# Optimization experiments

Hardware: AMD Instinct MI355X
Metric: run time of the kernel (lower is better)

The kernel has to match this reference:

```python
import jax, jax.numpy as jnp
import numpy as np

ALPHA = 1000.0  # softmin temperature from the original module


def setup_inputs() -> dict:
    key = jax.random.key(0)
    ks = jax.random.split(key, 10)
    B, D, H, E, K = 8192, 784, 256, 32, 512
    s = 0.05  # small init scale to keep activations/distances numerically sane
    return {
        "x": jax.random.normal(ks[0], (B, D), jnp.float32),
        "cluster_reps": jax.random.normal(ks[1], (K, E), jnp.float32),
        "W1": jax.random.normal(ks[2], (D, H), jnp.float32) * s,
        "b1": jnp.zeros((H,), jnp.float32),
        "W2": jax.random.normal(ks[3], (H, E), jnp.float32) * s,
        "b2": jnp.zeros((E,), jnp.float32),
        "W3": jax.random.normal(ks[4], (E, H), jnp.float32) * s,
        "b3": jnp.zeros((H,), jnp.float32),
        "W4": jax.random.normal(ks[5], (H, D), jnp.float32) * s,
        "b4": jnp.zeros((D,), jnp.float32),
    }


def reference(x, cluster_reps, W1, b1, W2, b2, W3, b3, W4, b4):
    # --- autoencoder: 2-layer MLP encoder / decoder ---
    h = jax.nn.relu(x @ W1 + b1)            # [B, H]
    embeddings = h @ W2 + b2                # [B, E]
    h2 = jax.nn.relu(embeddings @ W3 + b3)  # [B, H]
    reconstruction = h2 @ W4 + b4           # [B, D]

    # --- squared distances to cluster reps: [B, K] ---
    diff = embeddings[:, None, :] - cluster_reps[None, :, :]  # [B, K, E]
    distances = jnp.sum(diff * diff, axis=2)                  # [B, K]

    # --- stable softmin-weighted distances ---
    min_dist = jnp.min(distances, axis=1, keepdims=True)       # [B, 1]
    exponentials = jnp.exp(-ALPHA * (distances - min_dist))    # [B, K]
    sum_exponentials = jnp.sum(exponentials, axis=1, keepdims=True)
    weighted_dists = distances * (exponentials / sum_exponentials)

    return (weighted_dists, distances, reconstruction, embeddings)
```

## Files before the change

### kernel.cpp

```cpp
#include <hip/hip_runtime.h>
#include <cstddef>

#define NB 8192
#define ND 784
#define NH 256
#define NE 32
#define NK 512
#define ALPHA_F 1000.0f

typedef _Float16 h8 __attribute__((ext_vector_type(8)));
typedef float f32x4 __attribute__((ext_vector_type(4)));

#define TW1 25
#define TN1 8
#define NBW1 200
#define TW4 8
#define TN4 25
#define NBW4 200
#define NBW2 8
#define NBW3 8

__global__ __launch_bounds__(256)
void prep4_kernel(const float* __restrict__ W1, _Float16* __restrict__ w1thi,
                  _Float16* __restrict__ w1tlo,
                  const float* __restrict__ W4, _Float16* __restrict__ w4thi,
                  _Float16* __restrict__ w4tlo,
                  const float* __restrict__ W2, _Float16* __restrict__ w2thi,
                  _Float16* __restrict__ w2tlo,
                  const float* __restrict__ W3, _Float16* __restrict__ w3thi,
                  _Float16* __restrict__ w3tlo) {
    __shared__ float tile[32][33];
    const int b   = blockIdx.x;
    const int tid = threadIdx.x;

    const float* W; _Float16 *hi, *lo; int K, N, kt, nt;
    if (b < NBW1) {
        W = W1; hi = w1thi; lo = w1tlo; K = ND; N = NH;
        kt = b % TW1; nt = b / TW1;
    } else if (b < NBW1 + NBW4) {
        const int bb = b - NBW1;
        W = W4; hi = w4thi; lo = w4tlo; K = NH; N = ND;
        kt = bb % TW4; nt = bb / TW4;
    } else if (b < NBW1 + NBW4 + NBW2) {
        W = W2; hi = w2thi; lo = w2tlo; K = NH; N = NE;
        kt = b - (NBW1 + NBW4); nt = 0;
    } else {
        W = W3; hi = w3thi; lo = w3tlo; K = NE; N = NH;
        kt = 0; nt = b - (NBW1 + NBW4 + NBW2);
    }
    const int k0 = kt * 32, n0 = nt * 32;
    const int row = tid >> 3, c4 = (tid & 7) * 4;
    #pragma unroll
    for (int j = 0; j < 4; ++j) {
        const int k = k0 + row, n = n0 + c4 + j;
        tile[row][c4 + j] = (k < K && n < N) ? W[(size_t)k * N + n] : 0.f;
    }
    __syncthreads();
    const int n = n0 + row;
    if (n < N) {
        #pragma unroll
        for (int j = 0; j < 4; ++j) {
            const int k = k0 + c4 + j;
            if (k < K) {
                float w = tile[c4 + j][row];
                _Float16 hh = (_Float16)w;
                float r = w - (float)hh;
                hi[(size_t)n * K + k] = hh;
                lo[(size_t)n * K + k] = (_Float16)(r * 2048.0f);
            }
        }
    }
}

#define HSTR 264

__global__ __launch_bounds__(1024, 4)
void mega_kernel(const float* __restrict__ x, const float* __restrict__ reps,
                 const _Float16* __restrict__ w1thi, const _Float16* __restrict__ w1tlo,
                 const _Float16* __restrict__ w2thi, const _Float16* __restrict__ w2tlo,
                 const _Float16* __restrict__ w3thi, const _Float16* __restrict__ w3tlo,
                 const _Float16* __restrict__ w4thi, const _Float16* __restrict__ w4tlo,
                 const float* __restrict__ b1, const float* __restrict__ b2,
                 const float* __restrict__ b3, const float* __restrict__ b4,
                 float* __restrict__ emb_g, float* __restrict__ recon_g,
                 float* __restrict__ dist_g, float* __restrict__ wout_g) {
    __shared__ __align__(16) unsigned char lds[135936];
    _Float16* R0h  = (_Float16*)lds;
    _Float16* sA   = (_Float16*)(lds + 81920);
    _Float16* hP   = (_Float16*)(lds + 92160);
    float*    es   = (float*)(lds + 125952);
    _Float16* eh   = (_Float16*)(lds + 130560);
    _Float16* el   = (_Float16*)(lds + 133120);
    float*    rmin = (float*)(lds + 135680);
    float*    rinv = (float*)(lds + 135808);

    const int tid  = threadIdx.x;
    const int lane = tid & 63;
    const int wv   = tid >> 6;
    const int li   = lane & 15;
    const int kq   = (lane >> 4) * 8;
    const int quad = lane >> 4;
    const int r0   = blockIdx.x * 32;

    const float c1 = 1.0f / 2048.0f;
    const float c2 = c1 * c1;

    {
        _Float16* sBhi = R0h;
        _Float16* sBlo = R0h + 2 * 256 * 40;
        _Float16* sAhi = sA;
        _Float16* sAlo = sA + 2 * 32 * 40;
        const int aro  = tid >> 2;
        const int ak   = (tid & 3) * 8;
        const int brow = tid >> 2;
        const int bk   = (tid & 3) * 8;
        const float*    pA  = x + (size_t)(r0 + aro) * ND;
        const _Float16* pBh = w1thi + (size_t)brow * ND;
        const _Float16* pBl = w1tlo + (size_t)brow * ND;

        float araw[8];
        h8 rbh, rbl;

        auto pf = [&](int s) {
            if (tid < 128) {
                const int k = s * 32 + ak;
                if (k + 8 <= ND) {
                    f32x4 v0 = *(const f32x4*)(pA + k);
                    f32x4 v1 = *(const f32x4*)(pA + k + 4);
                    #pragma unroll
                    for (int j = 0; j < 4; ++j) {
                        araw[j] = v0[j]; araw[4 + j] = v1[j];
                    }
                } else {
                    #pragma unroll
                    for (int j = 0; j < 8; ++j) araw[j] = 0.f;
                }
            }
            const int kb = s * 32 + bk;
            rbh = (kb + 8 <= ND) ? *(const h8*)(pBh + kb) : (h8){};
            rbl = (kb + 8 <= ND) ? *(const h8*)(pBl + kb) : (h8){};
        };
        auto cm = [&](int buf) {
            if (tid < 128) {
                h8 hi, lo;
                #pragma unroll
                for (int j = 0; j < 8; ++j) {
                    float v = araw[j];
                    _Float16 hh = (_Float16)v;
                    hi[j] = hh;
                    lo[j] = (_Float16)((v - (float)hh) * 2048.0f);
                }
                *(h8*)&sAhi[buf * 32 * 40 + aro * 40 + ak] = hi;
                *(h8*)&sAlo[buf * 32 * 40 + aro * 40 + ak] = lo;
            }
            *(h8*)&sBhi[buf * 256 * 40 + brow * 40 + bk] = rbh;
            *(h8*)&sBlo[buf * 256 * 40 + brow * 40 + bk] = rbl;
        };

        pf(0); cm(0); pf(1);
        __syncthreads();

        f32x4 a0[2] = {}, a1[2] = {}, a2[2] = {};
        for (int s = 0; s < 25; ++s) {
            const int buf = s & 1;
            h8 fah[2], fal[2];
            #pragma unroll
            for (int mt = 0; mt < 2; ++mt) {
                const int ao = buf * 32 * 40 + (mt * 16 + li) * 40 + kq;
                fah[mt] = *(const h8*)&sAhi[ao];
                fal[mt] = *(const h8*)&sAlo[ao];
            }
            const int bo = buf * 256 * 40 + (wv * 16 + li) * 40 + kq;
            h8 fbh = *(const h8*)&sBhi[bo];
            h8 fbl = *(const h8*)&sBlo[bo];
            #pragma unroll
            for (int mt = 0; mt < 2; ++mt) {
                a0[mt] = __builtin_amdgcn_mfma_f32_16x16x32_f16(fah[mt], fbh, a0[mt], 0, 0, 0);
                a1[mt] = __builtin_amdgcn_mfma_f32_16x16x32_f16(fah[mt], fbl, a1[mt], 0, 0, 0);
                a1[mt] = __builtin_amdgcn_mfma_f32_16x16x32_f16(fal[mt], fbh, a1[mt], 0, 0, 0);
                a2[mt] = __builtin_amdgcn_mfma_f32_16x16x32_f16(fal[mt], fbl, a2[mt], 0, 0, 0);
            }
            if (s + 1 < 25) { cm((s + 1) & 1); if (s + 2 < 25) pf(s + 2); }
            __syncthreads();
        }
        _Float16* hhi = hP;
        _Float16* hlo = hP + 32 * HSTR;
        const int n = wv * 16 + li;
        const float bv = b1[n];
        #pragma unroll
        for (int mt = 0; mt < 2; ++mt)
            #pragma unroll
            for (int r = 0; r < 4; ++r) {
                const int m = mt * 16 + quad * 4 + r;
                float v = a0[mt][r] + c1 * a1[mt][r] + c2 * a2[mt][r] + bv;
                v = fmaxf(v, 0.f);
                _Float16 t = (_Float16)v;
                hhi[m * HSTR + n] = t;
                hlo[m * HSTR + n] = (_Float16)((v - (float)t) * 2048.0f);
            }
    }
    __syncthreads();

    {
        _Float16* w2h = R0h;
        _Float16* w2l = R0h + 32 * HSTR;
        const int row = tid >> 5, off = (tid & 31) * 8;
        *(h8*)&w2h[row * HSTR + off] = *(const h8*)(w2thi + row * 256 + off);
        *(h8*)&w2l[row * HSTR + off] = *(const h8*)(w2tlo + row * 256 + off);
    }
    __syncthreads();
    if (wv < 4) {
        const int mt = wv >> 1, nt = wv & 1;
        _Float16* hhi = hP;
        _Float16* hlo = hP + 32 * HSTR;
        _Float16* w2h = R0h;
        _Float16* w2l = R0h + 32 * HSTR;
        f32x4 e0 = {}, e1 = {}, e2 = {};
        #pragma unroll
        for (int ks = 0; ks < 8; ++ks) {
            const int k = ks * 32 + kq;
            h8 ah = *(const h8*)&hhi[(mt * 16 + li) * HSTR + k];
            h8 al = *(const h8*)&hlo[(mt * 16 + li) * HSTR + k];
            h8 bh = *(const h8*)&w2h[(nt * 16 + li) * HSTR + k];
            h8 bl = *(const h8*)&w2l[(nt * 16 + li) * HSTR + k];
            e0 = __builtin_amdgcn_mfma_f32_16x16x32_f16(ah, bh, e0, 0, 0, 0);
            e1 = __builtin_amdgcn_mfma_f32_16x16x32_f16(ah, bl, e1, 0, 0, 0);
            e1 = __builtin_amdgcn_mfma_f32_16x16x32_f16(al, bh, e1, 0, 0, 0);
            e2 = __builtin_amdgcn_mfma_f32_16x16x32_f16(al, bl, e2, 0, 0, 0);
        }
        const int col = nt * 16 + li;
        const float bv = b2[col];
        #pragma unroll
        for (int r = 0; r < 4; ++r) {
            const int m = mt * 16 + quad * 4 + r;
            float v = e0[r] + c1 * e1[r] + c2 * e2[r] + bv;
            es[m * 36 + col] = v;
            _Float16 t = (_Float16)v;
            eh[m * 40 + col] = t;
            el[m * 40 + col] = (_Float16)((v - (float)t) * 2048.0f);
            emb_g[(size_t)(r0 + m) * NE + col] = v;
        }
    }
    __syncthreads();

    {
        _Float16* w3h = R0h;
        _Float16* w3l = R0h + 256 * 40;
        const int row = tid >> 2, off = (tid & 3) * 8;
        *(h8*)&w3h[row * 40 + off] = *(const h8*)(w3thi + row * 32 + off);
        *(h8*)&w3l[row * 40 + off] = *(const h8*)(w3tlo + row * 32 + off);
    }
    __syncthreads();
    {
        _Float16* w3h  = R0h;
        _Float16* w3l  = R0h + 256 * 40;
        _Float16* h2h  = hP;
        _Float16* h2l  = hP + 32 * HSTR;
        h8 ah[2], al[2];
        #pragma unroll
        for (int mt = 0; mt < 2; ++mt) {
            ah[mt] = *(const h8*)&eh[(mt * 16 + li) * 40 + kq];
            al[mt] = *(const h8*)&el[(mt * 16 + li) * 40 + kq];
        }
        const int col = wv * 16 + li;
        h8 bh = *(const h8*)&w3h[col * 40 + kq];
        h8 bl = *(const h8*)&w3l[col * 40 + kq];
        const float bv = b3[col];
        #pragma unroll
        for (int mt = 0; mt < 2; ++mt) {
            f32x4 q0 = {}, q1 = {}, q2 = {};
            q0 = __builtin_amdgcn_mfma_f32_16x16x32_f16(ah[mt], bh, q0, 0, 0, 0);
            q1 = __builtin_amdgcn_mfma_f32_16x16x32_f16(ah[mt], bl, q1, 0, 0, 0);
            q1 = __builtin_amdgcn_mfma_f32_16x16x32_f16(al[mt], bh, q1, 0, 0, 0);
            q2 = __builtin_amdgcn_mfma_f32_16x16x32_f16(al[mt], bl, q2, 0, 0, 0);
            #pragma unroll
            for (int r = 0; r < 4; ++r) {
                const int m = mt * 16 + quad * 4 + r;
                float v = q0[r] + c1 * q1[r] + c2 * q2[r] + bv;
                v = fmaxf(v, 0.f);
                _Float16 t = (_Float16)v;
                h2h[m * HSTR + col] = t;
                h2l[m * HSTR + col] = (_Float16)((v - (float)t) * 2048.0f);
            }
        }
    }
    __syncthreads();

    {
        _Float16* sBhi = R0h;
        _Float16* sBlo = R0h + 4 * 128 * 40;
        _Float16* h2h  = hP;
        _Float16* h2l  = hP + 32 * HSTR;
        const int mt  = wv >> 3;
        const int ntw = wv & 7;
        const int brow = tid >> 2;
        const int bk4  = (tid & 3) * 8;
        h8 rbh[2], rbl[2];
        auto pf = [&](int ss) {
            if (tid < 512 && ss < 56) {
                int rg = (ss >> 3) * 128 + brow;
                if (rg > ND - 1) rg = ND - 1;
                const int k = (ss & 7) * 32 + bk4;
                rbh[ss & 1] = *(const h8*)(w4thi + (size_t)rg * NH + k);
                rbl[ss & 1] = *(const h8*)(w4tlo + (size_t)rg * NH + k);
            }
        };
        auto cm = [&](int ss) {
            if (tid < 512 && ss < 56) {
                const int sl = ss & 3;
                *(h8*)&sBhi[sl * 128 * 40 + brow * 40 + bk4] = rbh[ss & 1];
                *(h8*)&sBlo[sl * 128 * 40 + brow * 40 + bk4] = rbl[ss & 1];
            }
        };
        pf(0); pf(1); cm(0); cm(1); pf(2); pf(3);
        __syncthreads();

        f32x4 q0 = {}, q1 = {};
        auto step = [&](int t) {
            const int sl = t & 3, ks = t & 7;
            const int bo = sl * 128 * 40 + (ntw * 16 + li) * 40 + kq;
            h8 fbh = *(const h8*)&sBhi[bo];
            h8 fbl = *(const h8*)&sBlo[bo];
            const int k = ks * 32 + kq;
            h8 ah = *(const h8*)&h2h[(mt * 16 + li) * HSTR + k];
            h8 al = *(const h8*)&h2l[(mt * 16 + li) * HSTR + k];
            q0 = __builtin_amdgcn_mfma_f32_16x16x32_f16(ah, fbh, q0, 0, 0, 0);
            q1 = __builtin_amdgcn_mfma_f32_16x16x32_f16(ah, fbl, q1, 0, 0, 0);
            q1 = __builtin_amdgcn_mfma_f32_16x16x32_f16(al, fbh, q1, 0, 0, 0);
            if (ks == 7) {
                const int n = (t >> 3) * 128 + ntw * 16 + li;
                if (n < ND) {
                    const float bv = b4[n];
                    #pragma unroll
                    for (int r = 0; r < 4; ++r) {
                        const int m = mt * 16 + quad * 4 + r;
                        recon_g[(size_t)(r0 + m) * ND + n] = q0[r] + c1 * q1[r] + bv;
                    }
                }
                q0 = {}; q1 = {};
            }
        };
        for (int ii = 0; ii < 28; ++ii) {
            const int s0 = ii * 2;
            step(s0);
            step(s0 + 1);
            cm(s0 + 2); cm(s0 + 3);
            pf(s0 + 4); pf(s0 + 5);
            __syncthreads();
        }
    }
    __syncthreads();

    {
        float* tr0 = (float*)lds;
        float* tr1 = (float*)(lds + 33280);
        const int half = tid >> 9;
        const int cl   = tid & 511;
        float* trh = half ? tr1 : tr0;
        const int rbase = half * 16;

        const float* rp = reps + (size_t)cl * NE;
        f32x4 rv[8];
        #pragma unroll
        for (int e4 = 0; e4 < 8; ++e4) rv[e4] = ((const f32x4*)rp)[e4];

        float d[16];
        #pragma unroll
        for (int r = 0; r < 16; ++r) {
            float a = 0.f;
            #pragma unroll
            for (int e4 = 0; e4 < 8; ++e4) {
                f32x4 ev = *(const f32x4*)&es[(rbase + r) * 36 + e4 * 4];
                #pragma unroll
                for (int j = 0; j < 4; ++j) {
                    float t = ev[j] - rv[e4][j];
                    a = fmaf(t, t, a);
                }
            }
            d[r] = a;
            trh[r * 520 + cl] = a;
        }
        __syncthreads();
        {
            const int w8 = wv & 7;
            #pragma unroll
            for (int p = 0; p < 2; ++p) {
                const int rl = w8 * 2 + p;
                float m = trh[rl * 520 + lane];
                #pragma unroll
                for (int j = 1; j < 8; ++j)
                    m = fminf(m, trh[rl * 520 + lane + 64 * j]);
                #pragma unroll
                for (int off = 32; off > 0; off >>= 1)
                    m = fminf(m, __shfl_xor(m, off, 64));
                if (lane == 0) rmin[rbase + rl] = m;
            }
        }
        __syncthreads();
        #pragma unroll
        for (int r = 0; r < 16; ++r)
            trh[r * 520 + cl] = expf(-ALPHA_F * (d[r] - rmin[rbase + r]));
        __syncthreads();
        {
            const int w8 = wv & 7;
            #pragma unroll
            for (int p = 0; p < 2; ++p) {
                const int rl = w8 * 2 + p;
                float s = trh[rl * 520 + lane];
                #pragma unroll
                for (int j = 1; j < 8; ++j)
                    s += trh[rl * 520 + lane + 64 * j];
                #pragma unroll
                for (int off = 32; off > 0; off >>= 1)
                    s += __shfl_xor(s, off, 64);
                if (lane == 0) rinv[rbase + rl] = 1.0f / s;
            }
        }
        __syncthreads();
        #pragma unroll
        for (int r = 0; r < 16; ++r) {
            const size_t row = (size_t)(r0 + rbase + r);
            const float ev = trh[r * 520 + cl];
            dist_g[row * NK + cl] = d[r];
            wout_g[row * NK + cl] = d[r] * (ev * rinv[rbase + r]);
        }
    }
}

__global__ __launch_bounds__(256)
void splitw2_kernel(const float* __restrict__ W1, _Float16* __restrict__ w1thi,
                    _Float16* __restrict__ w1tlo,
                    const float* __restrict__ W4, _Float16* __restrict__ w4thi,
                    _Float16* __restrict__ w4tlo) {
    const int b = blockIdx.x;
    const float* W; _Float16 *hi, *lo; int K, N, n;
    if (b < NH) { W = W1; hi = w1thi; lo = w1tlo; K = ND; N = NH; n = b; }
    else        { W = W4; hi = w4thi; lo = w4tlo; K = NH; N = ND; n = b - NH; }
    for (int k = threadIdx.x; k < K; k += 256) {
        float w = W[(size_t)k * N + n];
        _Float16 hh = (_Float16)w;
        float r = w - (float)hh;
        hi[(size_t)n * K + k] = hh;
        lo[(size_t)n * K + k] = (_Float16)(r * 2048.0f);
    }
}

template<int TERMS, bool RELU, bool SPLITA, int MT>
__global__ __launch_bounds__(256)
void mfma_gemm3(const float* __restrict__ Af32,
                const _Float16* __restrict__ Ahi_g,
                const _Float16* __restrict__ Alo_g,
                const _Float16* __restrict__ WThi,
                const _Float16* __restrict__ WTlo,
                const float* __restrict__ bias, float* __restrict__ C,
                int N, int K, int KS) {
    constexpr int BM  = MT * 32;
    constexpr int ACH = BM / 64;
    constexpr int AS  = BM * 40;
    constexpr int BS  = 64 * 40;
    __shared__ __align__(16) _Float16 smem[2 * BM * 40 * 2 + 2 * 64 * 40 * 2];
    _Float16* sAhi = smem;
    _Float16* sAlo = sAhi + 2 * BM * 40;
    _Float16* sBhi = sAlo + 2 * BM * 40;
    _Float16* sBlo = sBhi + 2 * 64 * 40;

    const int tid = threadIdx.x;
    const int bm  = blockIdx.x * BM;
    const int bn  = blockIdx.y * 64;

    const int arow = (ACH == 1) ? (tid >> 2) : (tid >> 1);
    const int ak   = (ACH == 1) ? ((tid & 3) * 8) : ((tid & 1) * 16);
    const int brow = tid >> 2;
    const int bk   = (tid & 3) * 8;

    const float*    pA32 = SPLITA ? Af32 + (size_t)(bm + arow) * K : nullptr;
    const _Float16* pAhi = SPLITA ? nullptr : Ahi_g + (size_t)(bm + arow) * K;
    const _Float16* pAlo = SPLITA ? nullptr : Alo_g + (size_t)(bm + arow) * K;
    int brow_g = bn + brow; if (brow_g > N - 1) brow_g = N - 1;
    const _Float16* pBhi = WThi + (size_t)brow_g * K;
    const _Float16* pBlo = WTlo + (size_t)brow_g * K;

    float araw[ACH * 8];
    h8 rahi[ACH], ralo[ACH];
    h8 rbhi, rblo;

    auto prefetch = [&](int s) {
        #pragma unroll
        for (int c = 0; c < ACH; ++c) {
            const int k = s * 32 + ak + c * 8;
            if (SPLITA) {
                if (k + 8 <= K) {
                    f32x4 v0 = *(const f32x4*)(pA32 + k);
                    f32x4 v1 = *(const f32x4*)(pA32 + k + 4);
                    #pragma unroll
                    for (int j = 0; j < 4; ++j) {
                        araw[c * 8 + j]     = v0[j];
                        araw[c * 8 + 4 + j] = v1[j];
                    }
                } else {
                    #pragma unroll
                    for (int j = 0; j < 8; ++j) araw[c * 8 + j] = 0.f;
                }
            } else {
                rahi[c] = (k + 8 <= K) ? *(const h8*)(pAhi + k) : (h8){};
                ralo[c] = (k + 8 <= K) ? *(const h8*)(pAlo + k) : (h8){};
            }
        }
        const int kb = s * 32 + bk;
        rbhi = (kb + 8 <= K) ? *(const h8*)(pBhi + kb) : (h8){};
        rblo = (kb + 8 <= K) ? *(const h8*)(pBlo + kb) : (h8){};
    };

    auto commit = [&](int buf) {
        #pragma unroll
        for (int c = 0; c < ACH; ++c) {
            h8 hi, lo;
            if (SPLITA) {
                #pragma unroll
                for (int j = 0; j < 8; ++j) {
                    float v = araw[c * 8 + j];
                    _Float16 hh = (_Float16)v;
                    hi[j] = hh;
                    lo[j] = (_Float16)((v - (float)hh) * 2048.0f);
                }
            } else { hi = rahi[c]; lo = ralo[c]; }
            *(h8*)&sAhi[buf * AS + arow * 40 + ak + c * 8] = hi;
            *(h8*)&sAlo[buf * AS + arow * 40 + ak + c * 8] = lo;
        }
        *(h8*)&sBhi[buf * BS + brow * 40 + bk] = rbhi;
        *(h8*)&sBlo[buf * BS + brow * 40 + bk] = rblo;
    };

    prefetch(0);
    commit(0);
    prefetch(1);
    __syncthreads();

    const int lane = tid & 63;
    const int wv   = tid >> 6;
    const int wm   = (wv >> 1) * (MT * 16);
    const int wn   = (wv & 1) * 32;
    const int li   = lane & 15;
    const int kq   = (lane >> 4) * 8;

    f32x4 acc0[MT][2] = {};
    f32x4 acc1[MT][2] = {};
    f32x4 acc2[MT][2] = {};

    for (int s = 0; s < KS; ++s) {
        const int buf = s & 1;
        h8 fahi[MT], falo[MT], fbhi[2], fblo[2];
        #pragma unroll
        for (int mt = 0; mt < MT; ++mt) {
            const int ao = buf * AS + (wm + mt * 16 + li) * 40 + kq;
            fahi[mt] = *(const h8*)&sAhi[ao];
            falo[mt] = *(const h8*)&sAlo[ao];
        }
        #pragma unroll
        for (int nt = 0; nt < 2; ++nt) {
            const int bo = buf * BS + (wn + nt * 16 + li) * 40 + kq;
            fbhi[nt] = *(const h8*)&sBhi[bo];
            fblo[nt] = *(const h8*)&sBlo[bo];
        }
        #pragma unroll
        for (int mt = 0; mt < MT; ++mt)
            #pragma unroll
            for (int nt = 0; nt < 2; ++nt) {
                acc0[mt][nt] = __builtin_amdgcn_mfma_f32_16x16x32_f16(
                    fahi[mt], fbhi[nt], acc0[mt][nt], 0, 0, 0);
                acc1[mt][nt] = __builtin_amdgcn_mfma_f32_16x16x32_f16(
                    fahi[mt], fblo[nt], acc1[mt][nt], 0, 0, 0);
                acc1[mt][nt] = __builtin_amdgcn_mfma_f32_16x16x32_f16(
                    falo[mt], fbhi[nt], acc1[mt][nt], 0, 0, 0);
                if (TERMS == 4)
                    acc2[mt][nt] = __builtin_amdgcn_mfma_f32_16x16x32_f16(
                        falo[mt], fblo[nt], acc2[mt][nt], 0, 0, 0);
            }
        if (s + 1 < KS) {
            commit((s + 1) & 1);
            if (s + 2 < KS) prefetch(s + 2);
        }
        __syncthreads();
    }

    const float c1 = 1.0f / 2048.0f;
    const float c2 = c1 * c1;
    const int quad = lane >> 4;
    #pragma unroll
    for (int nt = 0; nt < 2; ++nt) {
        const int n = bn + wn + nt * 16 + li;
        if (n < N) {
            const float bv = bias[n];
            #pragma unroll
            for (int mt = 0; mt < MT; ++mt) {
                #pragma unroll
                for (int r = 0; r < 4; ++r) {
                    const int m = bm + wm + mt * 16 + quad * 4 + r;
                    float v = acc0[mt][nt][r] + c1 * acc1[mt][nt][r];
                    if (TERMS == 4) v += c2 * acc2[mt][nt][r];
                    v += bv;
                    if (RELU) v = fmaxf(v, 0.f);
                    C[(size_t)m * N + n] = v;
                }
            }
        }
    }
}

__global__ __launch_bounds__(256)
void mid_kernel(const float* __restrict__ h, const float* __restrict__ W2,
                const float* __restrict__ b2, const float* __restrict__ W3,
                const float* __restrict__ b3, float* __restrict__ emb,
                _Float16* __restrict__ h2hi, _Float16* __restrict__ h2lo) {
    __shared__ float es[16][32];
    const int tid = threadIdx.x;
    const int r0  = blockIdx.x * 16;

    #pragma unroll
    for (int half = 0; half < 2; ++half) {
        const int o   = tid + half * 256;
        const int row = o >> 5;
        const int col = o & 31;
        const float* hrow = h + (size_t)(r0 + row) * NH;
        float acc0 = 0.f, acc1 = 0.f;
        #pragma unroll 4
        for (int k = 0; k < NH; k += 4) {
            float4 hv = *(const float4*)(hrow + k);
            acc0 = fmaf(hv.x, W2[(k + 0) * NE + col], acc0);
            acc1 = fmaf(hv.y, W2[(k + 1) * NE + col], acc1);
            acc0 = fmaf(hv.z, W2[(k + 2) * NE + col], acc0);
            acc1 = fmaf(hv.w, W2[(k + 3) * NE + col], acc1);
        }
        float v = acc0 + acc1 + b2[col];
        es[row][col] = v;
        emb[(size_t)r0 * NE + o] = v;
    }
    __syncthreads();

    const int col = tid;
    float acc[16];
    #pragma unroll
    for (int r = 0; r < 16; ++r) acc[r] = 0.f;
    #pragma unroll
    for (int k = 0; k < NE; ++k) {
        float w = W3[k * NH + col];
        #pragma unroll
        for (int r = 0; r < 16; ++r) acc[r] = fmaf(es[r][k], w, acc[r]);
    }
    const float bb = b3[col];
    #pragma unroll
    for (int r = 0; r < 16; ++r) {
        float v = acc[r] + bb;
        v = v > 0.f ? v : 0.f;
        _Float16 hh = (_Float16)v;
        float rr = v - (float)hh;
        h2hi[(size_t)(r0 + r) * NH + col] = hh;
        h2lo[(size_t)(r0 + r) * NH + col] = (_Float16)(rr * 2048.0f);
    }
}

__global__ __launch_bounds__(512, 4)
void dist_kernel(const float* __restrict__ emb, const float* __restrict__ reps,
                 float* __restrict__ dist, float* __restrict__ wout) {
    __shared__ float es[8][32];
    __shared__ float tr[8][520];
    __shared__ float rmin[8];
    __shared__ float rinv[8];

    const int tid = threadIdx.x;
    const int r0  = blockIdx.x * 8;

    if (tid < 256) es[tid >> 5][tid & 31] = emb[(size_t)r0 * NE + tid];

    const float* rp = reps + (size_t)tid * NE;
    f32x4 rv[8];
    #pragma unroll
    for (int e4 = 0; e4 < 8; ++e4) rv[e4] = ((const f32x4*)rp)[e4];
    __syncthreads();

    float d[8];
    #pragma unroll
    for (int r = 0; r < 8; ++r) {
        float a = 0.f;
        #pragma unroll
        for (int e4 = 0; e4 < 8; ++e4) {
            f32x4 ev = *(const f32x4*)&es[r][e4 * 4];
            #pragma unroll
            for (int j = 0; j < 4; ++j) {
                float t = ev[j] - rv[e4][j];
                a = fmaf(t, t, a);
            }
        }
        d[r] = a;
    }

    const int lane = tid & 63;
    const int wv   = tid >> 6;

    #pragma unroll
    for (int r = 0; r < 8; ++r) tr[r][tid] = d[r];
    __syncthreads();
    {
        f32x4 a = *(const f32x4*)&tr[wv][lane * 8];
        f32x4 b = *(const f32x4*)&tr[wv][lane * 8 + 4];
        float m = fminf(fminf(fminf(a[0], a[1]), fminf(a[2], a[3])),
                        fminf(fminf(b[0], b[1]), fminf(b[2], b[3])));
        #pragma unroll
        for (int off = 32; off > 0; off >>= 1)
            m = fminf(m, __shfl_xor(m, off, 64));
        if (lane == 0) rmin[wv] = m;
    }
    __syncthreads();

    float e[8];
    #pragma unroll
    for (int r = 0; r < 8; ++r) {
        e[r] = expf(-ALPHA_F * (d[r] - rmin[r]));
        tr[r][tid] = e[r];
    }
    __syncthreads();
    {
        f32x4 a = *(const f32x4*)&tr[wv][lane * 8];
        f32x4 b = *(const f32x4*)&tr[wv][lane * 8 + 4];
        float s = ((a[0] + a[1]) + (a[2] + a[3])) +
                  ((b[0] + b[1]) + (b[2] + b[3]));
        #pragma unroll
        for (int off = 32; off > 0; off >>= 1)
            s += __shfl_xor(s, off, 64);
        if (lane == 0) rinv[wv] = 1.0f / s;
    }
    __syncthreads();

    #pragma unroll
    for (int r = 0; r < 8; ++r) {
        const size_t row = (size_t)(r0 + r);
        dist[row * NK + tid] = d[r];
        wout[row * NK + tid] = d[r] * (e[r] * rinv[r]);
    }
}

extern "C" void kernel_launch(void* const* d_in, const int* in_sizes, int n_in,
                              void* d_out, int out_size, void* d_ws, size_t ws_size,
                              hipStream_t stream) {
    const float* x    = (const float*)d_in[0];
    const float* reps = (const float*)d_in[1];
    const float* W1   = (const float*)d_in[2];
    const float* b1   = (const float*)d_in[3];
    const float* W2   = (const float*)d_in[4];
    const float* b2   = (const float*)d_in[5];
    const float* W3   = (const float*)d_in[6];
    const float* b3   = (const float*)d_in[7];
    const float* W4   = (const float*)d_in[8];
    const float* b4   = (const float*)d_in[9];

    float* out   = (float*)d_out;
    float* wout  = out;
    float* dist  = out + (size_t)NB * NK;
    float* recon = out + (size_t)2 * NB * NK;
    float* emb   = out + (size_t)2 * NB * NK + (size_t)NB * ND;

    const size_t nW14 = (size_t)ND * NH;
    const size_t nW23 = (size_t)NE * NH;
    const size_t wneed = (4 * nW14 + 4 * nW23) * sizeof(_Float16);

    if (d_ws != nullptr && ws_size >= wneed) {
        _Float16* w1thi = (_Float16*)d_ws;
        _Float16* w1tlo = w1thi + nW14;
        _Float16* w4thi = w1tlo + nW14;
        _Float16* w4tlo = w4thi + nW14;
        _Float16* w2thi = w4tlo + nW14;
        _Float16* w2tlo = w2thi + nW23;
        _Float16* w3thi = w2tlo + nW23;
        _Float16* w3tlo = w3thi + nW23;

        prep4_kernel<<<NBW1 + NBW4 + NBW2 + NBW3, 256, 0, stream>>>(
            W1, w1thi, w1tlo, W4, w4thi, w4tlo,
            W2, w2thi, w2tlo, W3, w3thi, w3tlo);

        mega_kernel<<<NB / 32, 1024, 0, stream>>>(
            x, reps, w1thi, w1tlo, w2thi, w2tlo, w3thi, w3tlo, w4thi, w4tlo,
            b1, b2, b3, b4, emb, recon, dist, wout);
    } else {
        float* h = dist;
        _Float16* h2hi  = (_Float16*)(dist + (size_t)NB * NH);
        _Float16* h2lo  = h2hi + (size_t)NB * NH;
        _Float16* w1thi = (_Float16*)wout;
        _Float16* w1tlo = w1thi + (size_t)NH * ND;
        _Float16* w4thi = w1tlo + (size_t)NH * ND;
        _Float16* w4tlo = w4thi + (size_t)ND * NH;

        splitw2_kernel<<<NH + ND, 256, 0, stream>>>(W1, w1thi, w1tlo,
                                                    W4, w4thi, w4tlo);
        mfma_gemm3<4, true, true, 2><<<dim3(128, 4), 256, 0, stream>>>(
            x, nullptr, nullptr, w1thi, w1tlo, b1, h, NH, ND, 25);
        mid_kernel<<<NB / 16, 256, 0, stream>>>(h, W2, b2, W3, b3,
                                                emb, h2hi, h2lo);
        mfma_gemm3<3, false, false, 4><<<dim3(64, 13), 256, 0, stream>>>(
            nullptr, h2hi, h2lo, w4thi, w4tlo, b4, recon, ND, NH, 8);
        dist_kernel<<<NB / 8, 512, 0, stream>>>(emb, reps, dist, wout);
    }
}
```

Baseline: 162.5 us.

## Replace padded LDS row strides with dense k-blocked 32-wide tiles

Shared-memory tiles switch from padded 40/264-element row strides to unpadded 32-element rows, with the hidden activations and W2 stored in k-blocked 32x32 chunks. The total LDS footprint shrinks and fragment reads become contiguous 1KB spans per wave. This risks different bank-conflict behaviour on scattered epilogue writes and on MFMA fragment loads that the padding previously avoided.

```diff
diff --git a/kernel.cpp b/kernel.cpp
--- a/kernel.cpp
+++ b/kernel.cpp
@@ -72,8 +72,6 @@
     }
 }
 
-#define HSTR 264
-
 __global__ __launch_bounds__(1024, 4)
 void mega_kernel(const float* __restrict__ x, const float* __restrict__ reps,
                  const _Float16* __restrict__ w1thi, const _Float16* __restrict__ w1tlo,
@@ -84,15 +82,14 @@
                  const float* __restrict__ b3, const float* __restrict__ b4,
                  float* __restrict__ emb_g, float* __restrict__ recon_g,
                  float* __restrict__ dist_g, float* __restrict__ wout_g) {
-    __shared__ __align__(16) unsigned char lds[135936];
+    __shared__ __align__(16) unsigned char lds[116480];
     _Float16* R0h  = (_Float16*)lds;
-    _Float16* sA   = (_Float16*)(lds + 81920);
-    _Float16* hP   = (_Float16*)(lds + 92160);
-    float*    es   = (float*)(lds + 125952);
-    _Float16* eh   = (_Float16*)(lds + 130560);
-    _Float16* el   = (_Float16*)(lds + 133120);
-    float*    rmin = (float*)(lds + 135680);
-    float*    rinv = (float*)(lds + 135808);
+    _Float16* sA   = (_Float16*)(lds + 66560);
+    _Float16* hP   = (_Float16*)(lds + 74752);
+    float*    es   = (float*)(lds + 107520);
+    _Float16* eP   = (_Float16*)(lds + 112128);
+    float*    rmin = (float*)(lds + 116224);
+    float*    rinv = (float*)(lds + 116352);
 
     const int tid  = threadIdx.x;
     const int lane = tid & 63;
@@ -107,9 +104,9 @@
 
     {
         _Float16* sBhi = R0h;
-        _Float16* sBlo = R0h + 2 * 256 * 40;
+        _Float16* sBlo = R0h + 2 * 8192;
         _Float16* sAhi = sA;
-        _Float16* sAlo = sA + 2 * 32 * 40;
+        _Float16* sAlo = sA + 2 * 1024;
         const int aro  = tid >> 2;
         const int ak   = (tid & 3) * 8;
         const int brow = tid >> 2;
@@ -150,11 +147,11 @@
                     hi[j] = hh;
                     lo[j] = (_Float16)((v - (float)hh) * 2048.0f);
                 }
-                *(h8*)&sAhi[buf * 32 * 40 + aro * 40 + ak] = hi;
-                *(h8*)&sAlo[buf * 32 * 40 + aro * 40 + ak] = lo;
-            }
-            *(h8*)&sBhi[buf * 256 * 40 + brow * 40 + bk] = rbh;
-            *(h8*)&sBlo[buf * 256 * 40 + brow * 40 + bk] = rbl;
+                *(h8*)&sAhi[buf * 1024 + aro * 32 + ak] = hi;
+                *(h8*)&sAlo[buf * 1024 + aro * 32 + ak] = lo;
+            }
+            *(h8*)&sBhi[buf * 8192 + brow * 32 + bk] = rbh;
+            *(h8*)&sBlo[buf * 8192 + brow * 32 + bk] = rbl;
         };
 
         pf(0); cm(0); pf(1);
@@ -166,11 +163,11 @@
             h8 fah[2], fal[2];
             #pragma unroll
             for (int mt = 0; mt < 2; ++mt) {
-                const int ao = buf * 32 * 40 + (mt * 16 + li) * 40 + kq;
+                const int ao = buf * 1024 + (mt * 16 + li) * 32 + kq;
                 fah[mt] = *(const h8*)&sAhi[ao];
                 fal[mt] = *(const h8*)&sAlo[ao];
             }
-            const int bo = buf * 256 * 40 + (wv * 16 + li) * 40 + kq;
+            const int bo = buf * 8192 + (wv * 16 + li) * 32 + kq;
             h8 fbh = *(const h8*)&sBhi[bo];
             h8 fbl = *(const h8*)&sBlo[bo];
             #pragma unroll
@@ -184,8 +181,9 @@
             __syncthreads();
         }
         _Float16* hhi = hP;
-        _Float16* hlo = hP + 32 * HSTR;
-        const int n = wv * 16 + li;
+        _Float16* hlo = hP + 8192;
+        const int n  = wv * 16 + li;
+        const int nb = n >> 5, nr = n & 31;
         const float bv = b1[n];
         #pragma unroll
         for (int mt = 0; mt < 2; ++mt)
@@ -195,34 +193,36 @@
                 float v = a0[mt][r] + c1 * a1[mt][r] + c2 * a2[mt][r] + bv;
                 v = fmaxf(v, 0.f);
                 _Float16 t = (_Float16)v;
-                hhi[m * HSTR + n] = t;
-                hlo[m * HSTR + n] = (_Float16)((v - (float)t) * 2048.0f);
+                hhi[nb * 1024 + m * 32 + nr] = t;
+                hlo[nb * 1024 + m * 32 + nr] = (_Float16)((v - (float)t) * 2048.0f);
             }
     }
     __syncthreads();
 
     {
         _Float16* w2h = R0h;
-        _Float16* w2l = R0h + 32 * HSTR;
-        const int row = tid >> 5, off = (tid & 31) * 8;
-        *(h8*)&w2h[row * HSTR + off] = *(const h8*)(w2thi + row * 256 + off);
-        *(h8*)&w2l[row * HSTR + off] = *(const h8*)(w2tlo + row * 256 + off);
+        _Float16* w2l = R0h + 8192;
+        const int col = tid >> 5;
+        const int k8  = tid & 31;
+        const int src = col * 256 + k8 * 8;
+        const int dst = (k8 >> 2) * 1024 + col * 32 + (k8 & 3) * 8;
+        *(h8*)&w2h[dst] = *(const h8*)(w2thi + src);
+        *(h8*)&w2l[dst] = *(const h8*)(w2tlo + src);
     }
     __syncthreads();
     if (wv < 4) {
         const int mt = wv >> 1, nt = wv & 1;
         _Float16* hhi = hP;
-        _Float16* hlo = hP + 32 * HSTR;
+        _Float16* hlo = hP + 8192;
         _Float16* w2h = R0h;
-        _Float16* w2l = R0h + 32 * HSTR;
+        _Float16* w2l = R0h + 8192;
         f32x4 e0 = {}, e1 = {}, e2 = {};
         #pragma unroll
         for (int ks = 0; ks < 8; ++ks) {
-            const int k = ks * 32 + kq;
-            h8 ah = *(const h8*)&hhi[(mt * 16 + li) * HSTR + k];
-            h8 al = *(const h8*)&hlo[(mt * 16 + li) * HSTR + k];
-            h8 bh = *(const h8*)&w2h[(nt * 16 + li) * HSTR + k];
-            h8 bl = *(const h8*)&w2l[(nt * 16 + li) * HSTR + k];
+            h8 ah = *(const h8*)&hhi[ks * 1024 + (mt * 16 + li) * 32 + kq];
+            h8 al = *(const h8*)&hlo[ks * 1024 + (mt * 16 + li) * 32 + kq];
+            h8 bh = *(const h8*)&w2h[ks * 1024 + (nt * 16 + li) * 32 + kq];
+            h8 bl = *(const h8*)&w2l[ks * 1024 + (nt * 16 + li) * 32 + kq];
             e0 = __builtin_amdgcn_mfma_f32_16x16x32_f16(ah, bh, e0, 0, 0, 0);
             e1 = __builtin_amdgcn_mfma_f32_16x16x32_f16(ah, bl, e1, 0, 0, 0);
             e1 = __builtin_amdgcn_mfma_f32_16x16x32_f16(al, bh, e1, 0, 0, 0);
@@ -230,14 +230,16 @@
         }
         const int col = nt * 16 + li;
         const float bv = b2[col];
+        _Float16* eh = eP;
+        _Float16* el = eP + 1024;
         #pragma unroll
         for (int r = 0; r < 4; ++r) {
             const int m = mt * 16 + quad * 4 + r;
             float v = e0[r] + c1 * e1[r] + c2 * e2[r] + bv;
             es[m * 36 + col] = v;
             _Float16 t = (_Float16)v;
-            eh[m * 40 + col] = t;
-            el[m * 40 + col] = (_Float16)((v - (float)t) * 2048.0f);
+            eh[m * 32 + col] = t;
+            el[m * 32 + col] = (_Float16)((v - (float)t) * 2048.0f);
             emb_g[(size_t)(r0 + m) * NE + col] = v;
         }
     }
@@ -245,27 +247,30 @@
 
     {
         _Float16* w3h = R0h;
-        _Float16* w3l = R0h + 256 * 40;
-        const int row = tid >> 2, off = (tid & 3) * 8;
-        *(h8*)&w3h[row * 40 + off] = *(const h8*)(w3thi + row * 32 + off);
-        *(h8*)&w3l[row * 40 + off] = *(const h8*)(w3tlo + row * 32 + off);
+        _Float16* w3l = R0h + 8192;
+        const int o = tid * 8;
+        *(h8*)&w3h[o] = *(const h8*)(w3thi + o);
+        *(h8*)&w3l[o] = *(const h8*)(w3tlo + o);
     }
     __syncthreads();
     {
         _Float16* w3h  = R0h;
-        _Float16* w3l  = R0h + 256 * 40;
+        _Float16* w3l  = R0h + 8192;
         _Float16* h2h  = hP;
-        _Float16* h2l  = hP + 32 * HSTR;
+        _Float16* h2l  = hP + 8192;
+        _Float16* eh   = eP;
+        _Float16* el   = eP + 1024;
         h8 ah[2], al[2];
         #pragma unroll
         for (int mt = 0; mt < 2; ++mt) {
-            ah[mt] = *(const h8*)&eh[(mt * 16 + li) * 40 + kq];
-            al[mt] = *(const h8*)&el[(mt * 16 + li) * 40 + kq];
+            ah[mt] = *(const h8*)&eh[(mt * 16 + li) * 32 + kq];
+            al[mt] = *(const h8*)&el[(mt * 16 + li) * 32 + kq];
         }
         const int col = wv * 16 + li;
-        h8 bh = *(const h8*)&w3h[col * 40 + kq];
-        h8 bl = *(const h8*)&w3l[col * 40 + kq];
+        h8 bh = *(const h8*)&w3h[col * 32 + kq];
+        h8 bl = *(const h8*)&w3l[col * 32 + kq];
         const float bv = b3[col];
+        const int cb = col >> 5, cr = col & 31;
         #pragma unroll
         for (int mt = 0; mt < 2; ++mt) {
             f32x4 q0 = {}, q1 = {}, q2 = {};
@@ -279,8 +284,8 @@
                 float v = q0[r] + c1 * q1[r] + c2 * q2[r] + bv;
                 v = fmaxf(v, 0.f);
                 _Float16 t = (_Float16)v;
-                h2h[m * HSTR + col] = t;
-                h2l[m * HSTR + col] = (_Float16)((v - (float)t) * 2048.0f);
+                h2h[cb * 1024 + m * 32 + cr] = t;
+                h2l[cb * 1024 + m * 32 + cr] = (_Float16)((v - (float)t) * 2048.0f);
             }
         }
     }
@@ -288,9 +293,9 @@
 
     {
         _Float16* sBhi = R0h;
-        _Float16* sBlo = R0h + 4 * 128 * 40;
+        _Float16* sBlo = R0h + 4 * 4096;
         _Float16* h2h  = hP;
-        _Float16* h2l  = hP + 32 * HSTR;
+        _Float16* h2l  = hP + 8192;
         const int mt  = wv >> 3;
         const int ntw = wv & 7;
         const int brow = tid >> 2;
@@ -308,8 +313,8 @@
         auto cm = [&](int ss) {
             if (tid < 512 && ss < 56) {
                 const int sl = ss & 3;
-                *(h8*)&sBhi[sl * 128 * 40 + brow * 40 + bk4] = rbh[ss & 1];
-                *(h8*)&sBlo[sl * 128 * 40 + brow * 40 + bk4] = rbl[ss & 1];
+                *(h8*)&sBhi[sl * 4096 + brow * 32 + bk4] = rbh[ss & 1];
+                *(h8*)&sBlo[sl * 4096 + brow * 32 + bk4] = rbl[ss & 1];
             }
         };
         pf(0); pf(1); cm(0); cm(1); pf(2); pf(3);
@@ -318,12 +323,12 @@
         f32x4 q0 = {}, q1 = {};
         auto step = [&](int t) {
             const int sl = t & 3, ks = t & 7;
-            const int bo = sl * 128 * 40 + (ntw * 16 + li) * 40 + kq;
+            const int bo = sl * 4096 + (ntw * 16 + li) * 32 + kq;
             h8 fbh = *(const h8*)&sBhi[bo];
             h8 fbl = *(const h8*)&sBlo[bo];
-            const int k = ks * 32 + kq;
-            h8 ah = *(const h8*)&h2h[(mt * 16 + li) * HSTR + k];
-            h8 al = *(const h8*)&h2l[(mt * 16 + li) * HSTR + k];
+            const int ao = ks * 1024 + (mt * 16 + li) * 32 + kq;
+            h8 ah = *(const h8*)&h2h[ao];
+            h8 al = *(const h8*)&h2l[ao];
             q0 = __builtin_amdgcn_mfma_f32_16x16x32_f16(ah, fbh, q0, 0, 0, 0);
             q1 = __builtin_amdgcn_mfma_f32_16x16x32_f16(ah, fbl, q1, 0, 0, 0);
             q1 = __builtin_amdgcn_mfma_f32_16x16x32_f16(al, fbh, q1, 0, 0, 0);
```

New measurement: 158.4 us. -2.5%, faster.
